# Performance work log

Hardware: AMD Instinct MI355X
Metric: run time of the kernel (lower is better)

## Reference

```python
import jax, jax.numpy as jnp
import numpy as np
from jax import lax

V, E, H, S, B = 32000, 150, 30, 128, 32
STDV = 1.0 / np.sqrt(30.0)


def setup_inputs() -> dict:
    key = jax.random.key(0)
    ks = jax.random.split(key, 9)
    u = lambda k, shape: jax.random.uniform(k, shape, jnp.float32, -STDV, STDV)
    return {
        "input_batch": jax.random.randint(ks[0], (S, B), 0, V),
        "embedding": u(ks[1], (V, E)),
        "W_ih_lr": u(ks[2], (E + H, H)),
        "b_ih_lr": u(ks[3], (1, H)),
        "W_ih_rl": u(ks[4], (E + H, H)),
        "b_ih_rl": u(ks[5], (1, H)),
        "W_ho": u(ks[6], (2 * H, V)),
        "b_ho": u(ks[7], (1, V)),
        "initial_hidden": u(ks[8], (1, H)),
    }


def reference(input_batch, embedding, W_ih_lr, b_ih_lr, W_ih_rl, b_ih_rl,
              W_ho, b_ho, initial_hidden):
    seq_len, batch = input_batch.shape
    emb = embedding[input_batch]  # (S, B, E)
    # original code detaches the initial hidden state (uses .data)
    init = jnp.broadcast_to(lax.stop_gradient(initial_hidden), (batch, initial_hidden.shape[1]))

    def step(W, b):
        def f(h, w):
            h_new = jnp.tanh(jnp.concatenate([w, h], axis=1) @ W + b)
            return h_new, h_new
        return f

    # forward (left-to-right): f_states[t] = hLR[t+1]
    _, f_states = lax.scan(step(W_ih_lr, b_ih_lr), init, emb)
    # backward (right-to-left) over reversed tokens: r_states[k] = hRL[S-1-k]
    _, r_states = lax.scan(step(W_ih_rl, b_ih_rl), init, emb[::-1])

    # prediction at i uses hLR[i] and hRL[i+1]
    hLR_used = jnp.concatenate([init[None], f_states[:-1]], axis=0)        # hLR[0..S-1]
    hRL_used = jnp.concatenate([r_states[:-1][::-1], init[None]], axis=0)  # hRL[1..S]

    h_cat = jnp.concatenate([hLR_used, hRL_used], axis=-1)  # (S, B, 2H)
    logits = jnp.einsum('sbh,hv->sbv', h_cat, W_ho) + b_ho  # (S, B, V)
    return jax.nn.log_softmax(logits, axis=-1)
```

## Files before the change

### kernel.cpp

```cpp
#include <hip/hip_runtime.h>

#define VSZ 32000
#define ESZ 150
#define HSZ 30
#define SSZ 128
#define BSZ 32
#define SB  4096
#define KP  64

typedef __attribute__((ext_vector_type(8))) short bf16x8;
typedef __attribute__((ext_vector_type(4))) float f32x4;
typedef __attribute__((ext_vector_type(8))) unsigned short u16x8;

static __device__ __forceinline__ unsigned short f2bf(float f) {
  unsigned int u = __float_as_uint(f);
  u += 0x7fffu + ((u >> 16) & 1u);
  return (unsigned short)(u >> 16);
}

static __device__ __forceinline__ float readlane_f(float v, int lane) {
  return __uint_as_float(__builtin_amdgcn_readlane(__float_as_uint(v), lane));
}

__global__ void k_zproj(const int* __restrict__ idx, const float* __restrict__ emb,
                        const float* __restrict__ Wlr, const float* __restrict__ blr,
                        const float* __restrict__ Wrl, const float* __restrict__ brl,
                        float* __restrict__ z) {
  __shared__ float erow[ESZ];
  int tb = blockIdx.x;
  int row = idx[tb];
  for (int i = threadIdx.x; i < ESZ; i += 64) erow[i] = emb[row * ESZ + i];
  __syncthreads();
  int lane = threadIdx.x;
  int j = lane & 31, dir = lane >> 5;
  if (j < HSZ) {
    const float* W = dir ? Wrl : Wlr;
    float acc = dir ? brl[j] : blr[j];
#pragma unroll 10
    for (int e = 0; e < ESZ; ++e) acc = fmaf(erow[e], W[e * HSZ + j], acc);
    z[(dir * SB + tb) * HSZ + j] = acc;
  }
}

__global__ void k_scan(const float* __restrict__ z, const float* __restrict__ Wlr,
                       const float* __restrict__ Wrl, const float* __restrict__ h0,
                       unsigned short* __restrict__ hcat) {
  int j = threadIdx.x;
  int chain = blockIdx.x;
  int dir = chain >> 5, b = chain & 31;
  const float* W = dir ? Wrl : Wlr;
  float w2[HSZ];
#pragma unroll
  for (int k = 0; k < HSZ; ++k) w2[k] = (j < HSZ) ? W[(ESZ + k) * HSZ + j] : 0.f;
  float h = (j < HSZ) ? h0[j] : 0.f;
  bool wr = (j < 32);
  int dim = (j < HSZ) ? dir * HSZ + j : (dir ? 60 : 62) + (j - 30);
  unsigned short padbits = (dim == 60) ? f2bf(1.0f) : (unsigned short)0;
  const float* zc = z + dir * (SB * HSZ) + b * HSZ + j;
  int te0 = dir ? (SSZ - 1) : 0;
  float zv = (j < HSZ) ? zc[te0 * (BSZ * HSZ)] : 0.f;
  for (int t = 0; t < SSZ; ++t) {
    int te = dir ? (SSZ - 1 - t) : t;
    float zn = 0.f;
    if (t < SSZ - 1) {
      int ten = dir ? (SSZ - 2 - t) : (t + 1);
      zn = (j < HSZ) ? zc[ten * (BSZ * HSZ)] : 0.f;
    }
    int r = te * BSZ + b;
    if (wr) hcat[r * KP + dim] = (j < HSZ) ? f2bf(h) : padbits;
    float a0 = zv, a1 = 0.f, a2 = 0.f, a3 = 0.f;
#pragma unroll
    for (int k = 0; k < 28; k += 4) {
      a0 = fmaf(readlane_f(h, k),     w2[k],     a0);
      a1 = fmaf(readlane_f(h, k + 1), w2[k + 1], a1);
      a2 = fmaf(readlane_f(h, k + 2), w2[k + 2], a2);
      a3 = fmaf(readlane_f(h, k + 3), w2[k + 3], a3);
    }
    a0 = fmaf(readlane_f(h, 28), w2[28], a0);
    a1 = fmaf(readlane_f(h, 29), w2[29], a1);
    float x = (a0 + a1) + (a2 + a3);
    float e = __expf(2.0f * x);
    h = 1.0f - __fdividef(2.0f, e + 1.0f);
    zv = zn;
  }
}

__global__ void k_wprep(const float* __restrict__ Who, const float* __restrict__ bho,
                        unsigned short* __restrict__ Wbt) {
  int v = blockIdx.x * 256 + threadIdx.x;
  int kq = blockIdx.y;
  u16x8 pack;
#pragma unroll
  for (int i = 0; i < 8; ++i) {
    int k = kq * 8 + i;
    float val = (k < 60) ? Who[k * VSZ + v] : ((k == 60) ? bho[v] : 0.f);
    pack[i] = f2bf(val);
  }
  *(u16x8*)&Wbt[v * KP + kq * 8] = pack;
}

__global__ void k_sumexp(const unsigned short* __restrict__ hcat,
                         const unsigned short* __restrict__ Wbt,
                         float* __restrict__ part) {
  int mb = blockIdx.x, nb = blockIdx.y;
  int wave = threadIdx.x >> 6, lane = threadIdx.x & 63;
  int g = lane >> 4, c = lane & 15;
  int rbase = mb * 128 + wave * 32;
  bf16x8 bfr[2][2];
#pragma unroll
  for (int rg = 0; rg < 2; ++rg)
#pragma unroll
    for (int ks = 0; ks < 2; ++ks)
      bfr[rg][ks] = *(const bf16x8*)&hcat[(rbase + rg * 16 + c) * KP + ks * 32 + g * 8];
  float se[2] = {0.f, 0.f};
  int c0 = nb * 2000;
  for (int nt = 0; nt < 125; ++nt) {
    int ct = c0 + nt * 16;
    bf16x8 a0 = *(const bf16x8*)&Wbt[(ct + c) * KP + g * 8];
    bf16x8 a1 = *(const bf16x8*)&Wbt[(ct + c) * KP + 32 + g * 8];
#pragma unroll
    for (int rg = 0; rg < 2; ++rg) {
      f32x4 acc = {0.f, 0.f, 0.f, 0.f};
      acc = __builtin_amdgcn_mfma_f32_16x16x32_bf16(a0, bfr[rg][0], acc, 0, 0, 0);
      acc = __builtin_amdgcn_mfma_f32_16x16x32_bf16(a1, bfr[rg][1], acc, 0, 0, 0);
      se[rg] += (__expf(acc[0]) + __expf(acc[1])) + (__expf(acc[2]) + __expf(acc[3]));
    }
  }
#pragma unroll
  for (int rg = 0; rg < 2; ++rg) {
    se[rg] += __shfl_xor(se[rg], 16);
    se[rg] += __shfl_xor(se[rg], 32);
  }
  if (g == 0) {
#pragma unroll
    for (int rg = 0; rg < 2; ++rg)
      part[(rbase + rg * 16 + c) * 16 + nb] = se[rg];
  }
}

__global__ void k_writeout(const unsigned short* __restrict__ hcat,
                           const unsigned short* __restrict__ Wbt,
                           const float* __restrict__ part,
                           float* __restrict__ out) {
  __shared__ float Lsh[128];
  int mb = blockIdx.x, nb = blockIdx.y;
  int tid = threadIdx.x;
  if (tid < 128) {
    const float* p = &part[(mb * 128 + tid) * 16];
    float s = 0.f;
#pragma unroll
    for (int k = 0; k < 16; ++k) s += p[k];
    Lsh[tid] = logf(s);
  }
  __syncthreads();
  int wave = tid >> 6, lane = tid & 63;
  int g = lane >> 4, c = lane & 15;
  int rbase = mb * 128 + wave * 32;
  bf16x8 bfr[2][2];
#pragma unroll
  for (int rg = 0; rg < 2; ++rg)
#pragma unroll
    for (int ks = 0; ks < 2; ++ks)
      bfr[rg][ks] = *(const bf16x8*)&hcat[(rbase + rg * 16 + c) * KP + ks * 32 + g * 8];
  float L[2];
#pragma unroll
  for (int rg = 0; rg < 2; ++rg) L[rg] = Lsh[wave * 32 + rg * 16 + c];
  int c0 = nb * 2000;
  for (int nt = 0; nt < 125; ++nt) {
    int ct = c0 + nt * 16;
    bf16x8 a0 = *(const bf16x8*)&Wbt[(ct + c) * KP + g * 8];
    bf16x8 a1 = *(const bf16x8*)&Wbt[(ct + c) * KP + 32 + g * 8];
#pragma unroll
    for (int rg = 0; rg < 2; ++rg) {
      f32x4 acc = {0.f, 0.f, 0.f, 0.f};
      acc = __builtin_amdgcn_mfma_f32_16x16x32_bf16(a0, bfr[rg][0], acc, 0, 0, 0);
      acc = __builtin_amdgcn_mfma_f32_16x16x32_bf16(a1, bfr[rg][1], acc, 0, 0, 0);
      f32x4 v;
#pragma unroll
      for (int i = 0; i < 4; ++i) v[i] = acc[i] - L[rg];
      *(f32x4*)&out[(rbase + rg * 16 + c) * VSZ + ct + g * 4] = v;
    }
  }
}

extern "C" void kernel_launch(void* const* d_in, const int* in_sizes, int n_in,
                              void* d_out, int out_size, void* d_ws, size_t ws_size,
                              hipStream_t stream) {
  (void)in_sizes; (void)n_in; (void)out_size; (void)ws_size;
  const int*   idx = (const int*)d_in[0];
  const float* emb = (const float*)d_in[1];
  const float* Wlr = (const float*)d_in[2];
  const float* blr = (const float*)d_in[3];
  const float* Wrl = (const float*)d_in[4];
  const float* brl = (const float*)d_in[5];
  const float* Who = (const float*)d_in[6];
  const float* bho = (const float*)d_in[7];
  const float* h0  = (const float*)d_in[8];
  float* out = (float*)d_out;

  char* ws = (char*)d_ws;
  float*          z    = (float*)(ws + 0);
  unsigned short* hcat = (unsigned short*)(ws + 983040);
  unsigned short* Wbt  = (unsigned short*)(ws + 1507328);
  float*          part = (float*)(ws + 5603328);

  k_zproj<<<SB, 64, 0, stream>>>(idx, emb, Wlr, blr, Wrl, brl, z);
  k_scan<<<64, 64, 0, stream>>>(z, Wlr, Wrl, h0, hcat);
  k_wprep<<<dim3(125, 8), 256, 0, stream>>>(Who, bho, Wbt);
  k_sumexp<<<dim3(32, 16), 256, 0, stream>>>(hcat, Wbt, part);
  k_writeout<<<dim3(32, 16), 256, 0, stream>>>(hcat, Wbt, part, out);
}
```

Before: 316.2 us.

## Stage logits tile in LDS for coalesced row writes and halve rows per wave

The writeout kernel now puts each wave's 16x256 logit tile into shared memory and writes it back as full contiguous 1 KB row segments, replacing scattered 16-byte stores spread across 16 rows. Each wave also handles 16 rows instead of 32, so the grid doubles and both GEMM kernels get more blocks. This aims at the write bandwidth of the 524 MB output, which dominates. In exchange it uses about 66 KB of LDS per block, which limits occupancy, and it loads W twice as often across blocks.

```diff
diff --git a/kernel.cpp b/kernel.cpp
--- a/kernel.cpp
+++ b/kernel.cpp
@@ -7,6 +7,7 @@
 #define BSZ 32
 #define SB  4096
 #define KP  64
+#define LPITCH 260
 
 typedef __attribute__((ext_vector_type(8))) short bf16x8;
 typedef __attribute__((ext_vector_type(4))) float f32x4;
@@ -99,54 +100,43 @@
   *(u16x8*)&Wbt[v * KP + kq * 8] = pack;
 }
 
-__global__ void k_sumexp(const unsigned short* __restrict__ hcat,
-                         const unsigned short* __restrict__ Wbt,
-                         float* __restrict__ part) {
+__global__ __launch_bounds__(256) void k_sumexp(
+    const unsigned short* __restrict__ hcat,
+    const unsigned short* __restrict__ Wbt,
+    float* __restrict__ part) {
   int mb = blockIdx.x, nb = blockIdx.y;
   int wave = threadIdx.x >> 6, lane = threadIdx.x & 63;
   int g = lane >> 4, c = lane & 15;
-  int rbase = mb * 128 + wave * 32;
-  bf16x8 bfr[2][2];
-#pragma unroll
-  for (int rg = 0; rg < 2; ++rg)
-#pragma unroll
-    for (int ks = 0; ks < 2; ++ks)
-      bfr[rg][ks] = *(const bf16x8*)&hcat[(rbase + rg * 16 + c) * KP + ks * 32 + g * 8];
-  float se[2] = {0.f, 0.f};
+  int row0 = mb * 64 + wave * 16;
+  bf16x8 b0f = *(const bf16x8*)&hcat[(row0 + c) * KP + g * 8];
+  bf16x8 b1f = *(const bf16x8*)&hcat[(row0 + c) * KP + 32 + g * 8];
+  float se = 0.f;
   int c0 = nb * 2000;
   for (int nt = 0; nt < 125; ++nt) {
     int ct = c0 + nt * 16;
     bf16x8 a0 = *(const bf16x8*)&Wbt[(ct + c) * KP + g * 8];
     bf16x8 a1 = *(const bf16x8*)&Wbt[(ct + c) * KP + 32 + g * 8];
-#pragma unroll
-    for (int rg = 0; rg < 2; ++rg) {
-      f32x4 acc = {0.f, 0.f, 0.f, 0.f};
-      acc = __builtin_amdgcn_mfma_f32_16x16x32_bf16(a0, bfr[rg][0], acc, 0, 0, 0);
-      acc = __builtin_amdgcn_mfma_f32_16x16x32_bf16(a1, bfr[rg][1], acc, 0, 0, 0);
-      se[rg] += (__expf(acc[0]) + __expf(acc[1])) + (__expf(acc[2]) + __expf(acc[3]));
-    }
-  }
-#pragma unroll
-  for (int rg = 0; rg < 2; ++rg) {
-    se[rg] += __shfl_xor(se[rg], 16);
-    se[rg] += __shfl_xor(se[rg], 32);
-  }
-  if (g == 0) {
-#pragma unroll
-    for (int rg = 0; rg < 2; ++rg)
-      part[(rbase + rg * 16 + c) * 16 + nb] = se[rg];
-  }
-}
-
-__global__ void k_writeout(const unsigned short* __restrict__ hcat,
-                           const unsigned short* __restrict__ Wbt,
-                           const float* __restrict__ part,
-                           float* __restrict__ out) {
-  __shared__ float Lsh[128];
+    f32x4 acc = {0.f, 0.f, 0.f, 0.f};
+    acc = __builtin_amdgcn_mfma_f32_16x16x32_bf16(a0, b0f, acc, 0, 0, 0);
+    acc = __builtin_amdgcn_mfma_f32_16x16x32_bf16(a1, b1f, acc, 0, 0, 0);
+    se += (__expf(acc[0]) + __expf(acc[1])) + (__expf(acc[2]) + __expf(acc[3]));
+  }
+  se += __shfl_xor(se, 16);
+  se += __shfl_xor(se, 32);
+  if (g == 0) part[(row0 + c) * 16 + nb] = se;
+}
+
+__global__ __launch_bounds__(256) void k_writeout(
+    const unsigned short* __restrict__ hcat,
+    const unsigned short* __restrict__ Wbt,
+    const float* __restrict__ part,
+    float* __restrict__ out) {
+  __shared__ float Lsh[64];
+  __shared__ float tile[4][16 * LPITCH];
   int mb = blockIdx.x, nb = blockIdx.y;
   int tid = threadIdx.x;
-  if (tid < 128) {
-    const float* p = &part[(mb * 128 + tid) * 16];
+  if (tid < 64) {
+    const float* p = &part[(mb * 64 + tid) * 16];
     float s = 0.f;
 #pragma unroll
     for (int k = 0; k < 16; ++k) s += p[k];
@@ -155,30 +145,38 @@
   __syncthreads();
   int wave = tid >> 6, lane = tid & 63;
   int g = lane >> 4, c = lane & 15;
-  int rbase = mb * 128 + wave * 32;
-  bf16x8 bfr[2][2];
-#pragma unroll
-  for (int rg = 0; rg < 2; ++rg)
-#pragma unroll
-    for (int ks = 0; ks < 2; ++ks)
-      bfr[rg][ks] = *(const bf16x8*)&hcat[(rbase + rg * 16 + c) * KP + ks * 32 + g * 8];
-  float L[2];
-#pragma unroll
-  for (int rg = 0; rg < 2; ++rg) L[rg] = Lsh[wave * 32 + rg * 16 + c];
+  int row0 = mb * 64 + wave * 16;
+  bf16x8 b0f = *(const bf16x8*)&hcat[(row0 + c) * KP + g * 8];
+  bf16x8 b1f = *(const bf16x8*)&hcat[(row0 + c) * KP + 32 + g * 8];
+  float L = Lsh[wave * 16 + c];
+  float* tl = tile[wave];
   int c0 = nb * 2000;
   for (int nt = 0; nt < 125; ++nt) {
     int ct = c0 + nt * 16;
     bf16x8 a0 = *(const bf16x8*)&Wbt[(ct + c) * KP + g * 8];
     bf16x8 a1 = *(const bf16x8*)&Wbt[(ct + c) * KP + 32 + g * 8];
-#pragma unroll
-    for (int rg = 0; rg < 2; ++rg) {
-      f32x4 acc = {0.f, 0.f, 0.f, 0.f};
-      acc = __builtin_amdgcn_mfma_f32_16x16x32_bf16(a0, bfr[rg][0], acc, 0, 0, 0);
-      acc = __builtin_amdgcn_mfma_f32_16x16x32_bf16(a1, bfr[rg][1], acc, 0, 0, 0);
-      f32x4 v;
-#pragma unroll
-      for (int i = 0; i < 4; ++i) v[i] = acc[i] - L[rg];
-      *(f32x4*)&out[(rbase + rg * 16 + c) * VSZ + ct + g * 4] = v;
+    f32x4 acc = {0.f, 0.f, 0.f, 0.f};
+    acc = __builtin_amdgcn_mfma_f32_16x16x32_bf16(a0, b0f, acc, 0, 0, 0);
+    acc = __builtin_amdgcn_mfma_f32_16x16x32_bf16(a1, b1f, acc, 0, 0, 0);
+    f32x4 v;
+#pragma unroll
+    for (int i = 0; i < 4; ++i) v[i] = acc[i] - L;
+    *(f32x4*)&tl[c * LPITCH + (nt & 15) * 16 + g * 4] = v;
+    if ((nt & 15) == 15) {
+      int cb = c0 + (nt >> 4) * 256;
+#pragma unroll 4
+      for (int r = 0; r < 16; ++r) {
+        f32x4 w = *(f32x4*)&tl[r * LPITCH + lane * 4];
+        *(f32x4*)&out[(row0 + r) * VSZ + cb + lane * 4] = w;
+      }
+    }
+  }
+  if (lane * 4 < 208) {
+    int cb = c0 + 1792;
+#pragma unroll 4
+    for (int r = 0; r < 16; ++r) {
+      f32x4 w = *(f32x4*)&tl[r * LPITCH + lane * 4];
+      *(f32x4*)&out[(row0 + r) * VSZ + cb + lane * 4] = w;
     }
   }
 }
@@ -207,6 +205,6 @@
   k_zproj<<<SB, 64, 0, stream>>>(idx, emb, Wlr, blr, Wrl, brl, z);
   k_scan<<<64, 64, 0, stream>>>(z, Wlr, Wrl, h0, hcat);
   k_wprep<<<dim3(125, 8), 256, 0, stream>>>(Who, bho, Wbt);
-  k_sumexp<<<dim3(32, 16), 256, 0, stream>>>(hcat, Wbt, part);
-  k_writeout<<<dim3(32, 16), 256, 0, stream>>>(hcat, Wbt, part, out);
-}
+  k_sumexp<<<dim3(64, 16), 256, 0, stream>>>(hcat, Wbt, part);
+  k_writeout<<<dim3(64, 16), 256, 0, stream>>>(hcat, Wbt, part, out);
+}
```

Result: slower. 435.5 us (+37.7%).

## Stage writeout tiles through swizzled LDS for coalesced nontemporal stores

Applied to the files above, without the earlier changes.

Restructures the log-softmax writeout kernel so each wave computes a 16x64 tile and stages it in an XOR-swizzled LDS slab. Each row is then written as contiguous 256-byte segments with nontemporal stores, replacing scattered 16-byte strided writes. Rows per block are halved and the grid doubled, which adds parallelism but doubles reloads of Wbt per row. This targets the write bandwidth of the 524 MB output, at the cost of extra LDS traffic and a leftover tail tile that still uses the old strided store.

```diff
diff --git a/kernel.cpp b/kernel.cpp
--- a/kernel.cpp
+++ b/kernel.cpp
@@ -138,15 +138,17 @@
   }
 }
 
-__global__ void k_writeout(const unsigned short* __restrict__ hcat,
-                           const unsigned short* __restrict__ Wbt,
-                           const float* __restrict__ part,
-                           float* __restrict__ out) {
-  __shared__ float Lsh[128];
+__global__ __launch_bounds__(256) void k_writeout(
+    const unsigned short* __restrict__ hcat,
+    const unsigned short* __restrict__ Wbt,
+    const float* __restrict__ part,
+    float* __restrict__ out) {
+  __shared__ float Lsh[64];
+  __shared__ float slab[4][16 * 64];
   int mb = blockIdx.x, nb = blockIdx.y;
   int tid = threadIdx.x;
-  if (tid < 128) {
-    const float* p = &part[(mb * 128 + tid) * 16];
+  if (tid < 64) {
+    const float* p = &part[(mb * 64 + tid) * 16];
     float s = 0.f;
 #pragma unroll
     for (int k = 0; k < 16; ++k) s += p[k];
@@ -155,31 +157,47 @@
   __syncthreads();
   int wave = tid >> 6, lane = tid & 63;
   int g = lane >> 4, c = lane & 15;
-  int rbase = mb * 128 + wave * 32;
-  bf16x8 bfr[2][2];
-#pragma unroll
-  for (int rg = 0; rg < 2; ++rg)
-#pragma unroll
-    for (int ks = 0; ks < 2; ++ks)
-      bfr[rg][ks] = *(const bf16x8*)&hcat[(rbase + rg * 16 + c) * KP + ks * 32 + g * 8];
-  float L[2];
-#pragma unroll
-  for (int rg = 0; rg < 2; ++rg) L[rg] = Lsh[wave * 32 + rg * 16 + c];
+  int row0 = mb * 64 + wave * 16;
+  bf16x8 b0f = *(const bf16x8*)&hcat[(row0 + c) * KP + g * 8];
+  bf16x8 b1f = *(const bf16x8*)&hcat[(row0 + c) * KP + 32 + g * 8];
+  float L = Lsh[wave * 16 + c];
+  float* tl = slab[wave];
   int c0 = nb * 2000;
-  for (int nt = 0; nt < 125; ++nt) {
-    int ct = c0 + nt * 16;
+  for (int gq = 0; gq < 31; ++gq) {
+    int ct0 = c0 + gq * 64;
+#pragma unroll
+    for (int t = 0; t < 4; ++t) {
+      int ct = ct0 + t * 16;
+      bf16x8 a0 = *(const bf16x8*)&Wbt[(ct + c) * KP + g * 8];
+      bf16x8 a1 = *(const bf16x8*)&Wbt[(ct + c) * KP + 32 + g * 8];
+      f32x4 acc = {0.f, 0.f, 0.f, 0.f};
+      acc = __builtin_amdgcn_mfma_f32_16x16x32_bf16(a0, b0f, acc, 0, 0, 0);
+      acc = __builtin_amdgcn_mfma_f32_16x16x32_bf16(a1, b1f, acc, 0, 0, 0);
+      f32x4 v;
+#pragma unroll
+      for (int i = 0; i < 4; ++i) v[i] = acc[i] - L;
+      int P = (t * 4 + g) ^ (c & 7);
+      *(f32x4*)&tl[c * 64 + P * 4] = v;
+    }
+#pragma unroll
+    for (int j = 0; j < 4; ++j) {
+      int rj = 4 * j + g;
+      int P = c ^ (rj & 7);
+      f32x4 w = *(f32x4*)&tl[rj * 64 + P * 4];
+      __builtin_nontemporal_store(w, (f32x4*)&out[(row0 + rj) * VSZ + ct0 + c * 4]);
+    }
+  }
+  {
+    int ct = c0 + 1984;
     bf16x8 a0 = *(const bf16x8*)&Wbt[(ct + c) * KP + g * 8];
     bf16x8 a1 = *(const bf16x8*)&Wbt[(ct + c) * KP + 32 + g * 8];
-#pragma unroll
-    for (int rg = 0; rg < 2; ++rg) {
-      f32x4 acc = {0.f, 0.f, 0.f, 0.f};
-      acc = __builtin_amdgcn_mfma_f32_16x16x32_bf16(a0, bfr[rg][0], acc, 0, 0, 0);
-      acc = __builtin_amdgcn_mfma_f32_16x16x32_bf16(a1, bfr[rg][1], acc, 0, 0, 0);
-      f32x4 v;
-#pragma unroll
-      for (int i = 0; i < 4; ++i) v[i] = acc[i] - L[rg];
-      *(f32x4*)&out[(rbase + rg * 16 + c) * VSZ + ct + g * 4] = v;
-    }
+    f32x4 acc = {0.f, 0.f, 0.f, 0.f};
+    acc = __builtin_amdgcn_mfma_f32_16x16x32_bf16(a0, b0f, acc, 0, 0, 0);
+    acc = __builtin_amdgcn_mfma_f32_16x16x32_bf16(a1, b1f, acc, 0, 0, 0);
+    f32x4 v;
+#pragma unroll
+    for (int i = 0; i < 4; ++i) v[i] = acc[i] - L;
+    *(f32x4*)&out[(row0 + c) * VSZ + ct + g * 4] = v;
   }
 }
 
@@ -208,5 +226,5 @@
   k_scan<<<64, 64, 0, stream>>>(z, Wlr, Wrl, h0, hcat);
   k_wprep<<<dim3(125, 8), 256, 0, stream>>>(Who, bho, Wbt);
   k_sumexp<<<dim3(32, 16), 256, 0, stream>>>(hcat, Wbt, part);
-  k_writeout<<<dim3(32, 16), 256, 0, stream>>>(hcat, Wbt, part, out);
-}
+  k_writeout<<<dim3(64, 16), 256, 0, stream>>>(hcat, Wbt, part, out);
+}
```

Measured after the change: 274.9 us. 1.15x faster.

## Stage writeout tiles through swizzled LDS for fully coalesced row stores

Applied to the files above, without the earlier changes.

The log-softmax writeout kernel now computes a 16-row by 256-column tile per step across four waves, stages it in shared memory with an XOR swizzle, and then writes each output row as contiguous 1 KB segments instead of scattered 64-byte pieces. The grid grows from 512 to 4096 blocks, each handling 16 rows and about 2048 columns, and the last column block handles the remainder. This targets write efficiency on the 524 MB output, which dominates runtime. In exchange it adds two barriers per step, 16 KB of LDS per block, and more repeated reads of the weight matrix because each block covers fewer rows.

```diff
diff --git a/kernel.cpp b/kernel.cpp
--- a/kernel.cpp
+++ b/kernel.cpp
@@ -138,48 +138,52 @@
   }
 }
 
-__global__ void k_writeout(const unsigned short* __restrict__ hcat,
-                           const unsigned short* __restrict__ Wbt,
-                           const float* __restrict__ part,
-                           float* __restrict__ out) {
-  __shared__ float Lsh[128];
+__global__ __launch_bounds__(256) void k_writeout(
+    const unsigned short* __restrict__ hcat,
+    const unsigned short* __restrict__ Wbt,
+    const float* __restrict__ part,
+    float* __restrict__ out) {
+  __shared__ float tile[16 * 256];
   int mb = blockIdx.x, nb = blockIdx.y;
-  int tid = threadIdx.x;
-  if (tid < 128) {
-    const float* p = &part[(mb * 128 + tid) * 16];
-    float s = 0.f;
-#pragma unroll
-    for (int k = 0; k < 16; ++k) s += p[k];
-    Lsh[tid] = logf(s);
-  }
-  __syncthreads();
-  int wave = tid >> 6, lane = tid & 63;
+  int wave = threadIdx.x >> 6, lane = threadIdx.x & 63;
   int g = lane >> 4, c = lane & 15;
-  int rbase = mb * 128 + wave * 32;
-  bf16x8 bfr[2][2];
-#pragma unroll
-  for (int rg = 0; rg < 2; ++rg)
-#pragma unroll
-    for (int ks = 0; ks < 2; ++ks)
-      bfr[rg][ks] = *(const bf16x8*)&hcat[(rbase + rg * 16 + c) * KP + ks * 32 + g * 8];
-  float L[2];
-#pragma unroll
-  for (int rg = 0; rg < 2; ++rg) L[rg] = Lsh[wave * 32 + rg * 16 + c];
-  int c0 = nb * 2000;
-  for (int nt = 0; nt < 125; ++nt) {
-    int ct = c0 + nt * 16;
-    bf16x8 a0 = *(const bf16x8*)&Wbt[(ct + c) * KP + g * 8];
-    bf16x8 a1 = *(const bf16x8*)&Wbt[(ct + c) * KP + 32 + g * 8];
-#pragma unroll
-    for (int rg = 0; rg < 2; ++rg) {
+  int row0 = mb * 16;
+  const float* p = &part[(row0 + c) * 16];
+  float s = 0.f;
+#pragma unroll
+  for (int k = 0; k < 16; ++k) s += p[k];
+  float L = logf(s);
+  bf16x8 b0f = *(const bf16x8*)&hcat[(row0 + c) * KP + g * 8];
+  bf16x8 b1f = *(const bf16x8*)&hcat[(row0 + c) * KP + 32 + g * 8];
+  int c0 = nb * 2048;
+  int nsteps = (nb == 15) ? 5 : 8;
+  for (int ss = 0; ss < nsteps; ++ss) {
+    int sbase = c0 + ss * 256;
+#pragma unroll
+    for (int t = 0; t < 4; ++t) {
+      int tt = wave * 4 + t;
+      int ct = sbase + tt * 16;
+      bf16x8 a0 = *(const bf16x8*)&Wbt[(ct + c) * KP + g * 8];
+      bf16x8 a1 = *(const bf16x8*)&Wbt[(ct + c) * KP + 32 + g * 8];
       f32x4 acc = {0.f, 0.f, 0.f, 0.f};
-      acc = __builtin_amdgcn_mfma_f32_16x16x32_bf16(a0, bfr[rg][0], acc, 0, 0, 0);
-      acc = __builtin_amdgcn_mfma_f32_16x16x32_bf16(a1, bfr[rg][1], acc, 0, 0, 0);
+      acc = __builtin_amdgcn_mfma_f32_16x16x32_bf16(a0, b0f, acc, 0, 0, 0);
+      acc = __builtin_amdgcn_mfma_f32_16x16x32_bf16(a1, b1f, acc, 0, 0, 0);
       f32x4 v;
 #pragma unroll
-      for (int i = 0; i < 4; ++i) v[i] = acc[i] - L[rg];
-      *(f32x4*)&out[(rbase + rg * 16 + c) * VSZ + ct + g * 4] = v;
-    }
+      for (int i = 0; i < 4; ++i) v[i] = acc[i] - L;
+      int G = tt * 4 + g;
+      int P = G ^ (c & 7);
+      *(f32x4*)&tile[c * 256 + P * 4] = v;
+    }
+    __syncthreads();
+#pragma unroll
+    for (int r = 0; r < 4; ++r) {
+      int R = wave * 4 + r;
+      int Pr = lane ^ (R & 7);
+      f32x4 w = *(f32x4*)&tile[R * 256 + Pr * 4];
+      *(f32x4*)&out[(row0 + R) * VSZ + sbase + lane * 4] = w;
+    }
+    __syncthreads();
   }
 }
 
@@ -208,5 +212,5 @@
   k_scan<<<64, 64, 0, stream>>>(z, Wlr, Wrl, h0, hcat);
   k_wprep<<<dim3(125, 8), 256, 0, stream>>>(Who, bho, Wbt);
   k_sumexp<<<dim3(32, 16), 256, 0, stream>>>(hcat, Wbt, part);
-  k_writeout<<<dim3(32, 16), 256, 0, stream>>>(hcat, Wbt, part, out);
-}
+  k_writeout<<<dim3(256, 16), 256, 0, stream>>>(hcat, Wbt, part, out);
+}
```

Result: no change. 310.7 us (-1.7%).
